# Optimization experiments

Measured on AMD Instinct MI355X. Metric: run time of the kernel, lower is better.

The kernel has to match this reference:

```python
import jax, jax.numpy as jnp
import numpy as np

N_PER_TYPE = 32000
N = 3 * N_PER_TYPE          # 96000 nodes
E = N * 16                  # 1,536,000 edges
H, D = 4, 8                 # num_heads, out_dim per head; hidden = 32
IN_DIMS = [128, 64, 32]
NEG_SLOPE = 0.2


def setup_inputs() -> dict:
    key = jax.random.key(0)
    ks = jax.random.split(key, 16)
    inp = {}
    # per-type raw features
    inp['x0'] = jax.random.normal(ks[0], (N_PER_TYPE, IN_DIMS[0]), jnp.float32)
    inp['x1'] = jax.random.normal(ks[1], (N_PER_TYPE, IN_DIMS[1]), jnp.float32)
    inp['x2'] = jax.random.normal(ks[2], (N_PER_TYPE, IN_DIMS[2]), jnp.float32)
    # per-type linear params (fc_list), scaled like kaiming-ish init
    inp['W0'] = jax.random.normal(ks[3], (IN_DIMS[0], H * D), jnp.float32) / np.sqrt(IN_DIMS[0])
    inp['b0'] = jnp.zeros((H * D,), jnp.float32)
    inp['W1'] = jax.random.normal(ks[4], (IN_DIMS[1], H * D), jnp.float32) / np.sqrt(IN_DIMS[1])
    inp['b1'] = jnp.zeros((H * D,), jnp.float32)
    inp['W2'] = jax.random.normal(ks[5], (IN_DIMS[2], H * D), jnp.float32) / np.sqrt(IN_DIMS[2])
    inp['b2'] = jnp.zeros((H * D,), jnp.float32)
    # GAT attention vectors a_l, a_r per head
    inp['attn_l'] = jax.random.normal(ks[6], (H, D), jnp.float32) / np.sqrt(D)
    inp['attn_r'] = jax.random.normal(ks[7], (H, D), jnp.float32) / np.sqrt(D)
    # node types laid out in contiguous blocks -> fixed-size index sets
    inp['type_mask'] = jnp.repeat(jnp.arange(3, dtype=jnp.int32), N_PER_TYPE)
    inp['idx0'] = jnp.arange(0, N_PER_TYPE, dtype=jnp.int32)
    inp['idx1'] = jnp.arange(N_PER_TYPE, 2 * N_PER_TYPE, dtype=jnp.int32)
    inp['idx2'] = jnp.arange(2 * N_PER_TYPE, 3 * N_PER_TYPE, dtype=jnp.int32)
    # random edge list
    inp['src'] = jax.random.randint(ks[8], (E,), 0, N, jnp.int32)
    inp['dst'] = jax.random.randint(ks[9], (E,), 0, N, jnp.int32)
    return inp


def reference(x0, x1, x2, W0, b0, W1, b1, W2, b2, attn_l, attn_r,
              idx0, idx1, idx2, src, dst, type_mask):
    # ---- type-masked per-type linear embed scattered into dense buffer ----
    t = jnp.zeros((N, H * D), x0.dtype)
    t = t.at[idx0].set(x0 @ W0 + b0)
    t = t.at[idx1].set(x1 @ W1 + b1)
    t = t.at[idx2].set(x2 @ W2 + b2)
    # (feat_drop is identity in eval mode)
    h = t.reshape(N, H, D)
    # ---- multi-head GAT attention ----
    el = jnp.einsum('nhd,hd->nh', h, attn_l)   # [N,H]
    er = jnp.einsum('nhd,hd->nh', h, attn_r)   # [N,H]
    e = jax.nn.leaky_relu(el[src] + er[dst], NEG_SLOPE)  # [E,H]
    # segment softmax over incoming edges of each dst node
    m = jax.ops.segment_max(e, dst, num_segments=N)      # [N,H]
    m = jnp.where(jnp.isfinite(m), m, 0.0)               # guard isolated nodes
    ex = jnp.exp(e - m[dst])                             # [E,H]
    s = jax.ops.segment_sum(ex, dst, num_segments=N)     # [N,H]
    alpha = ex / (s[dst] + 1e-9)                         # [E,H]
    # message aggregation
    msg = alpha[:, :, None] * h[src]                     # [E,H,D]
    out = jax.ops.segment_sum(msg, dst, num_segments=N)  # [N,H,D]
    # concat heads + ELU (standard intermediate-layer GAT activation)
    return jax.nn.elu(out).reshape(N, H * D)
```

## Files before the change

kernel.cpp:

```cpp
#include <hip/hip_runtime.h>
#include <hip/hip_bf16.h>
#include <math.h>

#define N_PER_TYPE 32000
#define NN (3 * N_PER_TYPE)
#define EDGES (NN * 16)
#define NHEAD 4
#define HD 32
#define NEG 0.2f
#define BINS 256
#define NPB (NN / BINS)
#define TILES 256
#define TPE (EDGES / TILES)
#define MAXBIN 8192
#define NB_EMBED 1500

typedef __attribute__((ext_vector_type(8))) short bf16x8;
typedef __attribute__((ext_vector_type(4))) float f32x4;

__device__ __forceinline__ unsigned packbf(float a, float b) {
    __hip_bfloat162 t = __float22bfloat162_rn(make_float2(a, b));
    return *reinterpret_cast<unsigned*>(&t);
}

__global__ __launch_bounds__(256) void embed_p1_kernel(
    const float* __restrict__ x0, const float* __restrict__ x1, const float* __restrict__ x2,
    const float* __restrict__ W0, const float* __restrict__ b0,
    const float* __restrict__ W1, const float* __restrict__ b1,
    const float* __restrict__ W2, const float* __restrict__ b2,
    const float* __restrict__ attn_l, const float* __restrict__ attn_r,
    __hip_bfloat16* __restrict__ h16, float* __restrict__ el, float* __restrict__ er,
    const int* __restrict__ dst, int* __restrict__ counts)
{
    int blk = blockIdx.x;
    int tid = threadIdx.x;

    if (blk >= NB_EMBED) {
        __shared__ int hist[BINS];
        int tile = blk - NB_EMBED;
        for (int i = tid; i < BINS; i += 256) hist[i] = 0;
        __syncthreads();
        int e0 = tile * TPE;
        for (int t = e0 + tid; t < e0 + TPE; t += 256)
            atomicAdd(&hist[dst[t] / NPB], 1);
        __syncthreads();
        for (int i = tid; i < BINS; i += 256) counts[tile * BINS + i] = hist[i];
        return;
    }

    __shared__ unsigned Wb[2048];
    __shared__ float hepi[64][33];

    int type = blk / 500;
    int nb = blk % 500;

    const float* x; const float* W; const float* bia; int in_dim;
    if (type == 0)      { x = x0; W = W0; bia = b0; in_dim = 128; }
    else if (type == 1) { x = x1; W = W1; bia = b1; in_dim = 64; }
    else                { x = x2; W = W2; bia = b2; in_dim = 32; }
    int KS = in_dim >> 5;

    int ndw = KS << 9;
    for (int i = tid; i < ndw; i += 256) {
        int d = i & 3, l = (i >> 2) & 63, sn = i >> 8;
        int s = sn >> 1, n = sn & 1;
        int k = (s << 5) + ((l >> 4) << 3) + (d << 1);
        int col = (n << 4) + (l & 15);
        Wb[i] = packbf(W[k * 32 + col], W[(k + 1) * 32 + col]);
    }
    __syncthreads();

    int wave = tid >> 6, lane = tid & 63;
    int node_l0 = wave * 16 + (lane & 15);
    const float* xrow = x + (size_t)(nb * 64 + node_l0) * in_dim;
    int kg = lane >> 4;

    f32x4 acc0 = {0.f, 0.f, 0.f, 0.f};
    f32x4 acc1 = {0.f, 0.f, 0.f, 0.f};

    for (int s = 0; s < KS; ++s) {
        int k0 = (s << 5) + (kg << 3);
        float4 xa = *(const float4*)(xrow + k0);
        float4 xb = *(const float4*)(xrow + k0 + 4);
        union { unsigned u[4]; bf16x8 v; } a;
        a.u[0] = packbf(xa.x, xa.y);
        a.u[1] = packbf(xa.z, xa.w);
        a.u[2] = packbf(xb.x, xb.y);
        a.u[3] = packbf(xb.z, xb.w);
        bf16x8 bfr0 = *(const bf16x8*)&Wb[((s * 2 + 0) * 64 + lane) * 4];
        bf16x8 bfr1 = *(const bf16x8*)&Wb[((s * 2 + 1) * 64 + lane) * 4];
        acc0 = __builtin_amdgcn_mfma_f32_16x16x32_bf16(a.v, bfr0, acc0, 0, 0, 0);
        acc1 = __builtin_amdgcn_mfma_f32_16x16x32_bf16(a.v, bfr1, acc1, 0, 0, 0);
    }

    int hrow = wave * 16 + ((lane >> 4) << 2);
    int hcol = lane & 15;
    #pragma unroll
    for (int r = 0; r < 4; ++r) {
        hepi[hrow + r][hcol]      = acc0[r];
        hepi[hrow + r][hcol + 16] = acc1[r];
    }
    __syncthreads();

    int node_e = tid >> 2, head = tid & 3;
    int node = blk * 64 + node_e;
    float4 al = *(const float4*)(attn_l + head * 8);
    float4 al2 = *(const float4*)(attn_l + head * 8 + 4);
    float4 ar = *(const float4*)(attn_r + head * 8);
    float4 ar2 = *(const float4*)(attn_r + head * 8 + 4);
    float bv = 0.0f;
    (void)bv;
    float hv[8];
    #pragma unroll
    for (int i = 0; i < 8; ++i) hv[i] = hepi[node_e][head * 8 + i] + bia[head * 8 + i];

    float elv = hv[0]*al.x + hv[1]*al.y + hv[2]*al.z + hv[3]*al.w
              + hv[4]*al2.x + hv[5]*al2.y + hv[6]*al2.z + hv[7]*al2.w;
    float erv = hv[0]*ar.x + hv[1]*ar.y + hv[2]*ar.z + hv[3]*ar.w
              + hv[4]*ar2.x + hv[5]*ar2.y + hv[6]*ar2.z + hv[7]*ar2.w;
    el[node * NHEAD + head] = elv;
    er[node * NHEAD + head] = erv;

    uint4 o;
    o.x = packbf(hv[0], hv[1]);
    o.y = packbf(hv[2], hv[3]);
    o.z = packbf(hv[4], hv[5]);
    o.w = packbf(hv[6], hv[7]);
    *reinterpret_cast<uint4*>((unsigned short*)h16 + (size_t)node * HD + head * 8) = o;
}

__global__ __launch_bounds__(256) void colscan_kernel(const int* __restrict__ counts,
                                                      int* __restrict__ colscan,
                                                      int* __restrict__ total) {
    __shared__ int s[256];
    int b = blockIdx.x, t = threadIdx.x;
    int v = counts[t * BINS + b];
    s[t] = v;
    __syncthreads();
    #pragma unroll
    for (int off = 1; off < 256; off <<= 1) {
        int tv = (t >= off) ? s[t - off] : 0;
        __syncthreads();
        s[t] += tv;
        __syncthreads();
    }
    colscan[t * BINS + b] = s[t] - v;
    if (t == 255) total[b] = s[255];
}

__global__ __launch_bounds__(256) void bstart_kernel(const int* __restrict__ total,
                                                     int* __restrict__ bstart) {
    __shared__ int s[256];
    int t = threadIdx.x;
    int v = total[t];
    s[t] = v;
    __syncthreads();
    #pragma unroll
    for (int off = 1; off < 256; off <<= 1) {
        int tv = (t >= off) ? s[t - off] : 0;
        __syncthreads();
        s[t] += tv;
        __syncthreads();
    }
    bstart[t] = s[t] - v;
    if (t == 255) bstart[256] = s[255];
}

__global__ __launch_bounds__(1024) void reorder_kernel(
    const int* __restrict__ src, const int* __restrict__ dst,
    const int* __restrict__ colscan, const int* __restrict__ bstart,
    unsigned* __restrict__ rec2)
{
    __shared__ int hist[BINS];
    __shared__ int sscan[BINS];
    __shared__ int prefix[BINS];
    __shared__ int offg[BINS];
    __shared__ unsigned sorted[TPE];
    __shared__ unsigned char binof[TPE];

    int tile = blockIdx.x, tid = threadIdx.x;
    for (int i = tid; i < BINS; i += 1024) hist[i] = 0;
    __syncthreads();

    int e0 = tile * TPE;
    unsigned rv[6]; int rb[6]; int rk[6]; int ne = 0;
    for (int t = e0 + tid; t < e0 + TPE; t += 1024) {
        int d = dst[t];
        int bin = d / NPB;
        int dl = d - bin * NPB;
        rv[ne] = ((unsigned)src[t] << 9) | (unsigned)dl;
        rb[ne] = bin;
        rk[ne] = atomicAdd(&hist[bin], 1);
        ++ne;
    }
    __syncthreads();

    if (tid < BINS) sscan[tid] = hist[tid];
    __syncthreads();
    #pragma unroll
    for (int off = 1; off < BINS; off <<= 1) {
        int tv = 0;
        if (tid < BINS && tid >= off) tv = sscan[tid - off];
        __syncthreads();
        if (tid < BINS) sscan[tid] += tv;
        __syncthreads();
    }
    if (tid < BINS) {
        int ex = sscan[tid] - hist[tid];
        prefix[tid] = ex;
        offg[tid] = bstart[tid] + colscan[tile * BINS + tid] - ex;
    }
    __syncthreads();

    #pragma unroll
    for (int q = 0; q < 6; ++q) if (q < ne) {
        int p = prefix[rb[q]] + rk[q];
        sorted[p] = rv[q];
        binof[p] = (unsigned char)rb[q];
    }
    __syncthreads();

    for (int j = tid; j < TPE; j += 1024) {
        int bin = binof[j];
        rec2[offg[bin] + j] = sorted[j];
    }
}

__global__ __launch_bounds__(1024) void place_kernel(
    const unsigned* __restrict__ rec2, const int* __restrict__ bstart,
    int* __restrict__ csr, int* __restrict__ start, int* __restrict__ deg)
{
    __shared__ int ncnt[NPB];
    __shared__ int noff[NPB];
    __shared__ int sc[512];
    __shared__ int ldscsr[MAXBIN];

    int k = blockIdx.x, tid = threadIdx.x;
    int bs = bstart[k];
    int be = bstart[k + 1];
    int cnt = be - bs;
    if (cnt > MAXBIN) cnt = MAXBIN;

    for (int i = tid; i < NPB; i += 1024) ncnt[i] = 0;
    __syncthreads();

    unsigned rsrc[8]; int rdl[8]; int rk8[8]; int ne = 0;
    for (int t = bs + tid; t < bs + cnt; t += 1024) {
        unsigned r = rec2[t];
        int dl = (int)(r & 511u);
        rsrc[ne] = r >> 9;
        rdl[ne] = dl;
        rk8[ne] = atomicAdd(&ncnt[dl], 1);
        ++ne;
    }
    __syncthreads();

    int v = 0;
    if (tid < 512) { v = (tid < NPB) ? ncnt[tid] : 0; sc[tid] = v; }
    __syncthreads();
    #pragma unroll
    for (int off = 1; off < 512; off <<= 1) {
        int tv = 0;
        if (tid < 512 && tid >= off) tv = sc[tid - off];
        __syncthreads();
        if (tid < 512) sc[tid] += tv;
        __syncthreads();
    }
    if (tid < NPB) {
        int ex = sc[tid] - v;
        noff[tid] = ex;
        start[k * NPB + tid] = bs + ex;
        deg[k * NPB + tid] = v;
    }
    __syncthreads();

    #pragma unroll
    for (int q = 0; q < 8; ++q) if (q < ne)
        ldscsr[noff[rdl[q]] + rk8[q]] = (int)rsrc[q];
    __syncthreads();

    for (int i = tid; i < cnt; i += 1024)
        csr[bs + i] = ldscsr[i];
}

__global__ __launch_bounds__(256) void agg_kernel(
    const int* __restrict__ csr, const int* __restrict__ start,
    const int* __restrict__ deg,
    const float* __restrict__ el, const float* __restrict__ er,
    const __hip_bfloat16* __restrict__ h16, float* __restrict__ out)
{
    int t = blockIdx.x * 256 + threadIdx.x;
    int node = t >> 4;
    int j = t & 15;
    int head = j >> 2;
    int hh = j & 3;
    int s0 = start[node];
    int len = deg[node];
    float er_s = er[node * NHEAD + hh];
    float acc0 = 0.f, acc1 = 0.f, den = 0.f;
    const unsigned* hp = (const unsigned*)h16;

    for (int base = 0; base < len; base += 16) {
        int cnt = len - base; if (cnt > 16) cnt = 16;
        int svl = (j < cnt) ? csr[s0 + base + j] : 0;
        for (int c = 0; c < cnt; c += 4) {
            int se = c + (j >> 2);
            int sv_s = __shfl(svl, se, 16);
            float xs = el[sv_s * NHEAD + hh] + er_s;
            xs = fmaxf(xs, NEG * xs);
            float exf = (se < cnt) ? __expf(xs) : 0.0f;
            #pragma unroll
            for (int i = 0; i < 4; ++i) {
                int sv = __shfl(svl, c + i, 16);
                float ex = __shfl(exf, (i << 2) + head, 16);
                unsigned p = hp[sv * 16 + j];
                den += ex;
                acc0 = fmaf(ex, __uint_as_float(p << 16),         acc0);
                acc1 = fmaf(ex, __uint_as_float(p & 0xffff0000u), acc1);
            }
        }
    }
    den += 1e-9f;
    float v0 = acc0 / den, v1 = acc1 / den;
    v0 = v0 > 0.f ? v0 : expm1f(v0);
    v1 = v1 > 0.f ? v1 : expm1f(v1);
    *reinterpret_cast<float2*>(out + node * HD + (j << 1)) = make_float2(v0, v1);
}

extern "C" void kernel_launch(void* const* d_in, const int* in_sizes, int n_in,
                              void* d_out, int out_size, void* d_ws, size_t ws_size,
                              hipStream_t stream) {
    const float* x0 = (const float*)d_in[0];
    const float* x1 = (const float*)d_in[1];
    const float* x2 = (const float*)d_in[2];
    const float* W0 = (const float*)d_in[3];
    const float* b0 = (const float*)d_in[4];
    const float* W1 = (const float*)d_in[5];
    const float* b1 = (const float*)d_in[6];
    const float* W2 = (const float*)d_in[7];
    const float* b2 = (const float*)d_in[8];
    const float* attn_l = (const float*)d_in[9];
    const float* attn_r = (const float*)d_in[10];
    const int* src = (const int*)d_in[15];
    const int* dst = (const int*)d_in[16];
    float* out = (float*)d_out;

    __hip_bfloat16* h16 = (__hip_bfloat16*)d_ws;
    float* el = (float*)(h16 + NN * HD);
    float* er = el + NN * NHEAD;
    int* deg     = (int*)(er + NN * NHEAD);
    int* start   = deg + NN;
    int* counts  = start + NN;
    int* colscan = counts + TILES * BINS;
    int* total   = colscan + TILES * BINS;
    int* bstart  = total + BINS;
    unsigned* rec2 = (unsigned*)(bstart + 260);
    int* csr     = (int*)(rec2 + EDGES);

    embed_p1_kernel<<<NB_EMBED + TILES, 256, 0, stream>>>(
        x0, x1, x2, W0, b0, W1, b1, W2, b2,
        attn_l, attn_r, h16, el, er, dst, counts);
    colscan_kernel<<<BINS, 256, 0, stream>>>(counts, colscan, total);
    bstart_kernel<<<1, 256, 0, stream>>>(total, bstart);
    reorder_kernel<<<TILES, 1024, 0, stream>>>(src, dst, colscan, bstart, rec2);
    place_kernel<<<BINS, 1024, 0, stream>>>(rec2, bstart, csr, start, deg);
    agg_kernel<<<NN * 16 / 256, 256, 0, stream>>>(csr, start, deg, el, er, h16, out);
}
```

Baseline: 68.57 us.

## Fuse CSR placement and attention aggregation into one kernel using LDS CSR

Merges the place and aggregation kernels so each bin's block builds its CSR in shared memory and then aggregates messages for its 375 nodes directly from LDS. This removes the global csr/start/deg writes and reads and one kernel launch. The cost is that aggregation now runs on only 256 blocks of 1024 threads with heavy LDS use, which can lower parallelism and occupancy relative to the separate 6000-block aggregation grid.

```diff
diff --git a/kernel.cpp b/kernel.cpp
--- a/kernel.cpp
+++ b/kernel.cpp
@@ -108,8 +108,6 @@
     float4 al2 = *(const float4*)(attn_l + head * 8 + 4);
     float4 ar = *(const float4*)(attn_r + head * 8);
     float4 ar2 = *(const float4*)(attn_r + head * 8 + 4);
-    float bv = 0.0f;
-    (void)bv;
     float hv[8];
     #pragma unroll
     for (int i = 0; i < 8; ++i) hv[i] = hepi[node_e][head * 8 + i] + bia[head * 8 + i];
@@ -226,9 +224,10 @@
     }
 }
 
-__global__ __launch_bounds__(1024) void place_kernel(
+__global__ __launch_bounds__(1024) void placeagg_kernel(
     const unsigned* __restrict__ rec2, const int* __restrict__ bstart,
-    int* __restrict__ csr, int* __restrict__ start, int* __restrict__ deg)
+    const float* __restrict__ el, const float* __restrict__ er,
+    const __hip_bfloat16* __restrict__ h16, float* __restrict__ out)
 {
     __shared__ int ncnt[NPB];
     __shared__ int noff[NPB];
@@ -266,12 +265,7 @@
         if (tid < 512) sc[tid] += tv;
         __syncthreads();
     }
-    if (tid < NPB) {
-        int ex = sc[tid] - v;
-        noff[tid] = ex;
-        start[k * NPB + tid] = bs + ex;
-        deg[k * NPB + tid] = v;
-    }
+    if (tid < NPB) noff[tid] = sc[tid] - v;
     __syncthreads();
 
     #pragma unroll
@@ -279,52 +273,49 @@
         ldscsr[noff[rdl[q]] + rk8[q]] = (int)rsrc[q];
     __syncthreads();
 
-    for (int i = tid; i < cnt; i += 1024)
-        csr[bs + i] = ldscsr[i];
-}
-
-__global__ __launch_bounds__(256) void agg_kernel(
-    const int* __restrict__ csr, const int* __restrict__ start,
-    const int* __restrict__ deg,
-    const float* __restrict__ el, const float* __restrict__ er,
-    const __hip_bfloat16* __restrict__ h16, float* __restrict__ out)
-{
-    int t = blockIdx.x * 256 + threadIdx.x;
-    int node = t >> 4;
-    int j = t & 15;
+    const unsigned* hp = (const unsigned*)h16;
+    int grp = tid >> 4;
+    int j = tid & 15;
     int head = j >> 2;
     int hh = j & 3;
-    int s0 = start[node];
-    int len = deg[node];
-    float er_s = er[node * NHEAD + hh];
-    float acc0 = 0.f, acc1 = 0.f, den = 0.f;
-    const unsigned* hp = (const unsigned*)h16;
-
-    for (int base = 0; base < len; base += 16) {
-        int cnt = len - base; if (cnt > 16) cnt = 16;
-        int svl = (j < cnt) ? csr[s0 + base + j] : 0;
-        for (int c = 0; c < cnt; c += 4) {
-            int se = c + (j >> 2);
-            int sv_s = __shfl(svl, se, 16);
-            float xs = el[sv_s * NHEAD + hh] + er_s;
-            xs = fmaxf(xs, NEG * xs);
-            float exf = (se < cnt) ? __expf(xs) : 0.0f;
-            #pragma unroll
-            for (int i = 0; i < 4; ++i) {
-                int sv = __shfl(svl, c + i, 16);
-                float ex = __shfl(exf, (i << 2) + head, 16);
-                unsigned p = hp[sv * 16 + j];
-                den += ex;
-                acc0 = fmaf(ex, __uint_as_float(p << 16),         acc0);
-                acc1 = fmaf(ex, __uint_as_float(p & 0xffff0000u), acc1);
+
+    #pragma unroll
+    for (int rnd = 0; rnd < 6; ++rnd) {
+        int dl = rnd * 64 + grp;
+        if (dl < NPB) {
+            int s0 = noff[dl];
+            int len = ncnt[dl];
+            int node = k * NPB + dl;
+            float er_s = er[node * NHEAD + hh];
+            float acc0 = 0.f, acc1 = 0.f, den = 0.f;
+
+            for (int base = 0; base < len; base += 16) {
+                int c16 = len - base; if (c16 > 16) c16 = 16;
+                int svl = (j < c16) ? ldscsr[s0 + base + j] : 0;
+                for (int c = 0; c < c16; c += 4) {
+                    int se = c + (j >> 2);
+                    int sv_s = __shfl(svl, se, 16);
+                    float xs = el[sv_s * NHEAD + hh] + er_s;
+                    xs = fmaxf(xs, NEG * xs);
+                    float exf = (se < c16) ? __expf(xs) : 0.0f;
+                    #pragma unroll
+                    for (int i = 0; i < 4; ++i) {
+                        int sv = __shfl(svl, c + i, 16);
+                        float ex = __shfl(exf, (i << 2) + head, 16);
+                        unsigned p = hp[sv * 16 + j];
+                        den += ex;
+                        acc0 = fmaf(ex, __uint_as_float(p << 16),         acc0);
+                        acc1 = fmaf(ex, __uint_as_float(p & 0xffff0000u), acc1);
+                    }
+                }
             }
+            den += 1e-9f;
+            float v0 = acc0 / den, v1 = acc1 / den;
+            v0 = v0 > 0.f ? v0 : expm1f(v0);
+            v1 = v1 > 0.f ? v1 : expm1f(v1);
+            *reinterpret_cast<float2*>(out + node * HD + (j << 1)) = make_float2(v0, v1);
         }
     }
-    den += 1e-9f;
-    float v0 = acc0 / den, v1 = acc1 / den;
-    v0 = v0 > 0.f ? v0 : expm1f(v0);
-    v1 = v1 > 0.f ? v1 : expm1f(v1);
-    *reinterpret_cast<float2*>(out + node * HD + (j << 1)) = make_float2(v0, v1);
 }
 
 extern "C" void kernel_launch(void* const* d_in, const int* in_sizes, int n_in,
@@ -348,14 +339,11 @@
     __hip_bfloat16* h16 = (__hip_bfloat16*)d_ws;
     float* el = (float*)(h16 + NN * HD);
     float* er = el + NN * NHEAD;
-    int* deg     = (int*)(er + NN * NHEAD);
-    int* start   = deg + NN;
-    int* counts  = start + NN;
+    int* counts  = (int*)(er + NN * NHEAD);
     int* colscan = counts + TILES * BINS;
     int* total   = colscan + TILES * BINS;
     int* bstart  = total + BINS;
     unsigned* rec2 = (unsigned*)(bstart + 260);
-    int* csr     = (int*)(rec2 + EDGES);
 
     embed_p1_kernel<<<NB_EMBED + TILES, 256, 0, stream>>>(
         x0, x1, x2, W0, b0, W1, b1, W2, b2,
@@ -363,6 +351,5 @@
     colscan_kernel<<<BINS, 256, 0, stream>>>(counts, colscan, total);
     bstart_kernel<<<1, 256, 0, stream>>>(total, bstart);
     reorder_kernel<<<TILES, 1024, 0, stream>>>(src, dst, colscan, bstart, rec2);
-    place_kernel<<<BINS, 1024, 0, stream>>>(rec2, bstart, csr, start, deg);
-    agg_kernel<<<NN * 16 / 256, 256, 0, stream>>>(csr, start, deg, el, er, h16, out);
-}
+    placeagg_kernel<<<BINS, 1024, 0, stream>>>(rec2, bstart, el, er, h16, out);
+}
```

After: 64.90 us. 5.4% less time.
